# Kernel optimization log

Hardware: AMD Instinct MI355X
Metric: run time of the kernel (lower is better)

Reference implementation:

```python
import jax, jax.numpy as jnp
import numpy as np

E, K = 8, 2
B, S, H = 8, 2048, 512
R0, R1, O = 256, 256, 512
T = B * S


def _make_routing(key):
    # Mixtral-style: top-k softmax weights [T, K] and one-hot mask [E, K, T]
    k1, k2 = jax.random.split(key)
    sel = jax.random.randint(k1, (T, K), 0, E)                      # selected expert per (token, slot)
    rw = jax.nn.softmax(jax.random.normal(k2, (T, K)), axis=-1)
    mask = jax.nn.one_hot(sel, E, dtype=jnp.bool_)                  # [T, K, E]
    mask = jnp.transpose(mask, (2, 1, 0))                           # [E, K, T]
    return mask, rw


def setup_inputs() -> dict:
    key = jax.random.key(0)
    ks = jax.random.split(key, 10)
    x = jax.random.normal(ks[0], (B, S, H), dtype=jnp.float32)
    m1, rw1 = _make_routing(ks[1])
    m2, rw2 = _make_routing(ks[2])
    m3, rw3 = _make_routing(ks[3])
    s = 0.02
    W1 = jax.random.normal(ks[4], (E, R0, H), dtype=jnp.float32) * s
    b1 = jnp.zeros((E, R0), dtype=jnp.float32)
    W2 = jax.random.normal(ks[5], (E, R1, R0), dtype=jnp.float32) * s
    b2 = jnp.zeros((E, R1), dtype=jnp.float32)
    W3 = jax.random.normal(ks[6], (E, O, R1), dtype=jnp.float32) * s
    b3 = jnp.zeros((E, O), dtype=jnp.float32)
    return {"x": x,
            "expert_mask1": m1, "expert_mask2": m2, "expert_mask3": m3,
            "routing_weights1": rw1, "routing_weights2": rw2, "routing_weights3": rw3,
            "W1": W1, "b1": b1, "W2": W2, "b2": b2, "W3": W3, "b3": b3}


def _moe_stage(h, mask, rw, W, b, act):
    # combine[e, t] = routing weight of token t for expert e (0 if not routed)
    cmb = jnp.einsum('ekt,tk->et', mask.astype(h.dtype), rw)
    acc0 = jnp.zeros((h.shape[0], W.shape[1]), dtype=h.dtype)

    def body(acc, ew):
        Wi, bi, ci = ew            # Wi: [out, in], bi: [out], ci: [T]
        out = h @ Wi.T + bi
        if act:
            out = jax.nn.relu(out)
        return acc + ci[:, None] * out, None

    acc, _ = jax.lax.scan(body, acc0, (W, b, cmb))
    return acc


def reference(x, expert_mask1, expert_mask2, expert_mask3,
              routing_weights1, routing_weights2, routing_weights3,
              W1, b1, W2, b2, W3, b3):
    bsz, seq, dim = x.shape
    h = x.reshape(-1, dim)                                          # [T, H]
    h = _moe_stage(h, expert_mask1, routing_weights1, W1, b1, act=False)   # [T, R0]
    h = _moe_stage(h, expert_mask2, routing_weights2, W2, b2, act=False)   # [T, R1]
    h = _moe_stage(h, expert_mask3, routing_weights3, W3, b3, act=True)    # relu on expert output, then combine
    out = jax.nn.relu(h.reshape(bsz, seq, -1))
    return out
```

## Files before the change

kernel.cpp:

```cpp
#include <hip/hip_runtime.h>

#define T_TOKENS 16384
#define CAP 12288
#define CNT_STRIDE 16

typedef unsigned short u16;
typedef unsigned int u32;
typedef __attribute__((ext_vector_type(8))) short short8;
typedef __attribute__((ext_vector_type(4))) float float4v;

__device__ __forceinline__ u16 f2b(float f) {
  unsigned u = __float_as_uint(f);
  u = (u + 0x7fffu + ((u >> 16) & 1u)) >> 16;
  return (u16)u;
}
__device__ __forceinline__ float b2f(u16 h) {
  return __uint_as_float(((unsigned)h) << 16);
}

__device__ __forceinline__ void gl_lds16(const u16* g, u16* l) {
  __builtin_amdgcn_global_load_lds((const __attribute__((address_space(1))) u32*)g,
                                   (__attribute__((address_space(3))) u32*)l, 16, 0, 0);
}

__global__ __launch_bounds__(256) void prep_kernel(
    const int* __restrict__ m1, const int* __restrict__ m2, const int* __restrict__ m3,
    const float* __restrict__ rw1, const float* __restrict__ rw2, const float* __restrict__ rw3,
    const float* __restrict__ W1, const float* __restrict__ W2, const float* __restrict__ W3,
    u16* __restrict__ Wb1, u16* __restrict__ Wb2, u16* __restrict__ Wb3,
    int* __restrict__ cnt, int* __restrict__ idxbuf, float* __restrict__ wgtbuf) {
  const int tid = threadIdx.x;
  const int bid = blockIdx.x;
  if (bid < 64) {
    __shared__ int lcnt[24];
    __shared__ int lbase[24];
    if (tid < 24) lcnt[tid] = 0;
    __syncthreads();
    const int t = bid * 256 + tid;
    const int* masks[3] = {m1, m2, m3};
    const float* rws[3] = {rw1, rw2, rw3};
    int expert[3][2], lpos[3][2];
#pragma unroll
    for (int s = 0; s < 3; ++s)
#pragma unroll
      for (int k = 0; k < 2; ++k) {
        int e = 0;
#pragma unroll
        for (int j = 0; j < 8; ++j)
          if (masks[s][(j * 2 + k) * T_TOKENS + t] != 0) e = j;
        expert[s][k] = e;
        lpos[s][k] = atomicAdd(&lcnt[s * 8 + e], 1);
      }
    __syncthreads();
    if (tid < 24) lbase[tid] = atomicAdd(&cnt[tid * CNT_STRIDE], lcnt[tid]);
    __syncthreads();
#pragma unroll
    for (int s = 0; s < 3; ++s)
#pragma unroll
      for (int k = 0; k < 2; ++k) {
        int e = expert[s][k];
        int p = lbase[s * 8 + e] + lpos[s][k];
        if (p < CAP) {
          idxbuf[(s * 8 + e) * CAP + p] = t * 2 + k;
          wgtbuf[(s * 8 + e) * CAP + p] = rws[s][t * 2 + k];
        }
      }
  } else {
    for (int j = bid - 64; j < 1280; j += 192) {
      int base = j * 2048 + tid * 8;
      const float* src; u16* dst; int off = base;
      if (base < 1048576) { src = W1; dst = Wb1; }
      else if (base < 1572864) { src = W2; dst = Wb2; off = base - 1048576; }
      else { src = W3; dst = Wb3; off = base - 1572864; }
      float4 a0 = *(const float4*)(src + off);
      float4 a1 = *(const float4*)(src + off + 4);
      short8 v;
      v[0] = (short)f2b(a0.x); v[1] = (short)f2b(a0.y);
      v[2] = (short)f2b(a0.z); v[3] = (short)f2b(a0.w);
      v[4] = (short)f2b(a1.x); v[5] = (short)f2b(a1.y);
      v[6] = (short)f2b(a1.z); v[7] = (short)f2b(a1.w);
      *(short8*)(dst + off) = v;
    }
  }
}

template <int KDIM, int NDIM_TOTAL, int SRC, int RELU>
__global__ __launch_bounds__(256, 2) void moe_gemm(
    const void* __restrict__ Asrc_, const u16* __restrict__ Wb, const float* __restrict__ bias,
    const int* __restrict__ cnt, const int* __restrict__ idxbuf, const float* __restrict__ wgtbuf,
    u16* __restrict__ outTmp) {
  __shared__ __align__(16) u16 As[128 * 64];
  __shared__ __align__(16) u16 Bs[256 * 64];
  __shared__ int rowTok[128];
  __shared__ float rowW[128];

  int b = blockIdx.x;
  int e = -1, row0 = 0, n_e = 0, accb = 0;
#pragma unroll
  for (int j = 0; j < 8; ++j) {
    int nj = cnt[j * CNT_STRIDE];
    nj = nj > CAP ? CAP : nj;
    int nb = (nj + 127) >> 7;
    if (e < 0 && b < accb + nb) { e = j; row0 = (b - accb) << 7; n_e = nj; }
    accb += nb;
  }
  if (e < 0) return;

  const int tid = threadIdx.x;
  if (tid < 128) {
    int g = row0 + tid;
    bool ok = g < n_e;
    rowTok[tid] = ok ? idxbuf[e * CAP + g] : 0;
    rowW[tid] = ok ? wgtbuf[e * CAP + g] : 0.f;
  }
  __syncthreads();

  const int nbase = blockIdx.y * 256;
  const int wv = tid >> 6, lane = tid & 63;
  const int lrow = lane & 15, lquad = lane >> 4;
  const int mh = wv >> 1, nh = wv & 1;

  const u16* Wbe = Wb + ((size_t)e * NDIM_TOTAL + nbase) * KDIM;

  const int lr = lane >> 3;
  const int lgl = (lane & 7) ^ lr;
  const u16* gB = Wbe + (size_t)(wv * 8 + lr) * KDIM + lgl * 8;
  u16* lB = &Bs[(wv * 8) * 64];

  const float* ga_f[4];
  const u16* ga_b[4];
  int awoff[4];
#pragma unroll
  for (int i = 0; i < 4; ++i) {
    int r = i * 32 + (tid >> 3);
    if (SRC == 0)
      ga_f[i] = (const float*)Asrc_ + (size_t)(rowTok[r] >> 1) * KDIM + (tid & 7) * 8;
    else
      ga_b[i] = (const u16*)Asrc_ + (size_t)(rowTok[r] >> 1) * 2 * KDIM + (tid & 7) * 8;
    awoff[i] = (r * 8 + ((tid & 7) ^ (r & 7))) * 8;
  }

  float4v acc[4][8];
#pragma unroll
  for (int mt = 0; mt < 4; ++mt)
#pragma unroll
    for (int nt = 0; nt < 8; ++nt) acc[mt][nt] = (float4v)0.f;

  for (int kb = 0; kb < KDIM; kb += 64) {
#pragma unroll
    for (int i = 0; i < 8; ++i)
      gl_lds16(gB + (size_t)i * 32 * KDIM + kb, lB + i * 32 * 64);
    if (SRC == 0) {
#pragma unroll
      for (int i = 0; i < 4; ++i) {
        float4 a0 = *(const float4*)(ga_f[i] + kb);
        float4 a1 = *(const float4*)(ga_f[i] + kb + 4);
        short8 v;
        v[0] = (short)f2b(a0.x); v[1] = (short)f2b(a0.y);
        v[2] = (short)f2b(a0.z); v[3] = (short)f2b(a0.w);
        v[4] = (short)f2b(a1.x); v[5] = (short)f2b(a1.y);
        v[6] = (short)f2b(a1.z); v[7] = (short)f2b(a1.w);
        *(short8*)&As[awoff[i]] = v;
      }
    } else {
#pragma unroll
      for (int i = 0; i < 4; ++i) {
        short8 v0 = *(const short8*)(ga_b[i] + kb);
        short8 v1 = *(const short8*)(ga_b[i] + kb + KDIM);
        short8 v;
#pragma unroll
        for (int jj = 0; jj < 8; ++jj)
          v[jj] = (short)f2b(b2f((u16)v0[jj]) + b2f((u16)v1[jj]));
        *(short8*)&As[awoff[i]] = v;
      }
    }
    __syncthreads();
#pragma unroll
    for (int ks = 0; ks < 64; ks += 32) {
      const int gb = ks >> 3;
      short8 af[4], bf[8];
#pragma unroll
      for (int mt = 0; mt < 4; ++mt) {
        int r = mh * 64 + mt * 16 + lrow;
        int p = (gb + lquad) ^ (lrow & 7);
        af[mt] = *(const short8*)&As[(r * 8 + p) * 8];
      }
#pragma unroll
      for (int nt = 0; nt < 8; ++nt) {
        int r = nh * 128 + nt * 16 + lrow;
        int p = (gb + lquad) ^ (lrow & 7);
        bf[nt] = *(const short8*)&Bs[(r * 8 + p) * 8];
      }
#pragma unroll
      for (int mt = 0; mt < 4; ++mt)
#pragma unroll
        for (int nt = 0; nt < 8; ++nt)
          acc[mt][nt] = __builtin_amdgcn_mfma_f32_16x16x32_bf16(af[mt], bf[nt], acc[mt][nt], 0, 0, 0);
    }
    __syncthreads();
  }

  float bv[8];
#pragma unroll
  for (int nt = 0; nt < 8; ++nt)
    bv[nt] = bias[e * NDIM_TOTAL + nbase + nh * 128 + nt * 16 + lrow];
#pragma unroll
  for (int mt = 0; mt < 4; ++mt)
#pragma unroll
    for (int i = 0; i < 4; ++i) {
      int m = mh * 64 + mt * 16 + lquad * 4 + i;
      if (row0 + m < n_e) {
        float w = rowW[m];
        size_t drow = (size_t)rowTok[m] * NDIM_TOTAL + nbase + nh * 128;
#pragma unroll
        for (int nt = 0; nt < 8; ++nt) {
          float v = acc[mt][nt][i] + bv[nt];
          if (RELU) v = fmaxf(v, 0.f);
          outTmp[drow + nt * 16 + lrow] = f2b(v * w);
        }
      }
    }
}

__global__ void finalize_kernel(const u16* __restrict__ tmp3, float* __restrict__ out) {
  int f = (blockIdx.x * 256 + threadIdx.x) * 8;
  int t = f >> 9;
  int o = f & 511;
  const u16* p = tmp3 + (size_t)t * 1024 + o;
  short8 v0 = *(const short8*)p;
  short8 v1 = *(const short8*)(p + 512);
  float4 r0, r1;
  r0.x = fmaxf(b2f((u16)v0[0]) + b2f((u16)v1[0]), 0.f);
  r0.y = fmaxf(b2f((u16)v0[1]) + b2f((u16)v1[1]), 0.f);
  r0.z = fmaxf(b2f((u16)v0[2]) + b2f((u16)v1[2]), 0.f);
  r0.w = fmaxf(b2f((u16)v0[3]) + b2f((u16)v1[3]), 0.f);
  r1.x = fmaxf(b2f((u16)v0[4]) + b2f((u16)v1[4]), 0.f);
  r1.y = fmaxf(b2f((u16)v0[5]) + b2f((u16)v1[5]), 0.f);
  r1.z = fmaxf(b2f((u16)v0[6]) + b2f((u16)v1[6]), 0.f);
  r1.w = fmaxf(b2f((u16)v0[7]) + b2f((u16)v1[7]), 0.f);
  *(float4*)(out + f) = r0;
  *(float4*)(out + f + 4) = r1;
}

extern "C" void kernel_launch(void* const* d_in, const int* in_sizes, int n_in,
                              void* d_out, int out_size, void* d_ws, size_t ws_size,
                              hipStream_t stream) {
  const float* x  = (const float*)d_in[0];
  const int* m1   = (const int*)d_in[1];
  const int* m2   = (const int*)d_in[2];
  const int* m3   = (const int*)d_in[3];
  const float* rw1 = (const float*)d_in[4];
  const float* rw2 = (const float*)d_in[5];
  const float* rw3 = (const float*)d_in[6];
  const float* W1 = (const float*)d_in[7];
  const float* b1 = (const float*)d_in[8];
  const float* W2 = (const float*)d_in[9];
  const float* b2 = (const float*)d_in[10];
  const float* W3 = (const float*)d_in[11];
  const float* b3 = (const float*)d_in[12];
  float* out = (float*)d_out;

  char* ws = (char*)d_ws;
  size_t off = 0;
  int* cnt = (int*)(ws + off); off += 24 * CNT_STRIDE * 4;
  u16* Wb1 = (u16*)(ws + off); off += (size_t)8 * 256 * 512 * 2;
  u16* Wb2 = (u16*)(ws + off); off += (size_t)8 * 256 * 256 * 2;
  u16* Wb3 = (u16*)(ws + off); off += (size_t)8 * 512 * 256 * 2;
  u16* tmp1 = (u16*)(ws + off); off += (size_t)T_TOKENS * 2 * 256 * 2;
  u16* tmp2 = (u16*)(ws + off); off += (size_t)T_TOKENS * 2 * 256 * 2;
  u16* tmp3 = (u16*)(ws + off); off += (size_t)T_TOKENS * 2 * 512 * 2;
  int* idxb = (int*)(ws + off); off += (size_t)3 * 8 * CAP * 4;
  float* wgtb = (float*)(ws + off); off += (size_t)3 * 8 * CAP * 4;

  hipMemsetAsync(cnt, 0, 24 * CNT_STRIDE * 4, stream);
  prep_kernel<<<256, 256, 0, stream>>>(m1, m2, m3, rw1, rw2, rw3, W1, W2, W3,
                                       Wb1, Wb2, Wb3, cnt, idxb, wgtb);

  moe_gemm<512, 256, 0, 0><<<dim3(264, 1), 256, 0, stream>>>(
      x, Wb1, b1, cnt + 0, idxb + 0, wgtb + 0, tmp1);
  moe_gemm<256, 256, 1, 0><<<dim3(264, 1), 256, 0, stream>>>(
      tmp1, Wb2, b2, cnt + 8 * CNT_STRIDE, idxb + 8 * CAP, wgtb + 8 * CAP, tmp2);
  moe_gemm<256, 512, 1, 1><<<dim3(264, 2), 256, 0, stream>>>(
      tmp2, Wb3, b3, cnt + 16 * CNT_STRIDE, idxb + 16 * CAP, wgtb + 16 * CAP, tmp3);

  finalize_kernel<<<4096, 256, 0, stream>>>(tmp3, out);
}
```

Measured before the change: 193.1 us.

## Fuse three MoE GEMM stages and finalize into one persistent kernel

Replaces the three per-stage GEMM launches and the finalize launch with a single persistent kernel of 264 blocks. The blocks loop over jobs and synchronize between stages with atomic grid barriers. This removes launch gaps and tail effects between kernels. In exchange it adds barrier spin cost and relies on all 264 blocks being co-resident, and stage 3 now runs its 2x jobs over only 264 blocks in a loop.

```diff
diff --git a/kernel.cpp b/kernel.cpp
--- a/kernel.cpp
+++ b/kernel.cpp
@@ -3,6 +3,7 @@
 #define T_TOKENS 16384
 #define CAP 12288
 #define CNT_STRIDE 16
+#define GRID_MEGA 264
 
 typedef unsigned short u16;
 typedef unsigned int u32;
@@ -21,6 +22,17 @@
 __device__ __forceinline__ void gl_lds16(const u16* g, u16* l) {
   __builtin_amdgcn_global_load_lds((const __attribute__((address_space(1))) u32*)g,
                                    (__attribute__((address_space(3))) u32*)l, 16, 0, 0);
+}
+
+__device__ __forceinline__ void grid_barrier(int* bar, int nblk) {
+  __syncthreads();
+  if (threadIdx.x == 0) {
+    __threadfence();
+    __hip_atomic_fetch_add(bar, 1, __ATOMIC_ACQ_REL, __HIP_MEMORY_SCOPE_AGENT);
+    while (__hip_atomic_load(bar, __ATOMIC_ACQUIRE, __HIP_MEMORY_SCOPE_AGENT) < nblk)
+      __builtin_amdgcn_s_sleep(8);
+  }
+  __syncthreads();
 }
 
 __global__ __launch_bounds__(256) void prep_kernel(
@@ -85,161 +97,168 @@
 }
 
 template <int KDIM, int NDIM_TOTAL, int SRC, int RELU>
-__global__ __launch_bounds__(256, 2) void moe_gemm(
-    const void* __restrict__ Asrc_, const u16* __restrict__ Wb, const float* __restrict__ bias,
-    const int* __restrict__ cnt, const int* __restrict__ idxbuf, const float* __restrict__ wgtbuf,
-    u16* __restrict__ outTmp) {
+__device__ void gemm_stage(const void* __restrict__ Asrc_, const u16* __restrict__ Wb,
+                           const float* __restrict__ bias, const int* __restrict__ cnt,
+                           const int* __restrict__ idxbuf, const float* __restrict__ wgtbuf,
+                           u16* __restrict__ outTmp, u16* As, u16* Bs, int* rowTok, float* rowW) {
+  constexpr int NB = NDIM_TOTAL / 256;
+  const int tid = threadIdx.x;
+  const int wv = tid >> 6, lane = tid & 63;
+  const int lrow = lane & 15, lquad = lane >> 4;
+  const int mh = wv >> 1, nh = wv & 1;
+  const int lr = lane >> 3, lgl = (lane & 7) ^ lr;
+
+  int n_arr[8], nb_arr[8], tot = 0;
+#pragma unroll
+  for (int j = 0; j < 8; ++j) {
+    int nj = cnt[j * CNT_STRIDE];
+    nj = nj > CAP ? CAP : nj;
+    n_arr[j] = nj;
+    nb_arr[j] = (nj + 127) >> 7;
+    tot += nb_arr[j];
+  }
+  const int njobs = tot * NB;
+
+  for (int job = blockIdx.x; job < njobs; job += gridDim.x) {
+    int rb = job, nbase = 0;
+    if (NB == 2 && job >= tot) { rb = job - tot; nbase = 256; }
+    int ee = 0, row0 = 0, n_e = 0, a = 0;
+#pragma unroll
+    for (int j = 0; j < 8; ++j) {
+      if (rb >= a && rb < a + nb_arr[j]) { ee = j; row0 = (rb - a) << 7; n_e = n_arr[j]; }
+      a += nb_arr[j];
+    }
+    if (tid < 128) {
+      int g = row0 + tid;
+      bool ok = g < n_e;
+      rowTok[tid] = ok ? idxbuf[ee * CAP + g] : 0;
+      rowW[tid] = ok ? wgtbuf[ee * CAP + g] : 0.f;
+    }
+    __syncthreads();
+
+    const u16* Wbe = Wb + ((size_t)ee * NDIM_TOTAL + nbase) * KDIM;
+    const u16* gB = Wbe + (size_t)(wv * 8 + lr) * KDIM + lgl * 8;
+
+    float4v acc[4][8];
+#pragma unroll
+    for (int mt = 0; mt < 4; ++mt)
+#pragma unroll
+      for (int nt = 0; nt < 8; ++nt) acc[mt][nt] = (float4v)0.f;
+
+    for (int kb = 0; kb < KDIM; kb += 64) {
+#pragma unroll
+      for (int i = 0; i < 8; ++i)
+        gl_lds16(gB + (size_t)i * 32 * KDIM + kb, &Bs[(wv * 8 + i * 32) * 64]);
+#pragma unroll
+      for (int i = 0; i < 4; ++i) {
+        int row = i * 32 + (tid >> 3), lg = tid & 7, ph = lg ^ (row & 7);
+        short8 v;
+        if (SRC == 0) {
+          const float* xp = (const float*)Asrc_ + (size_t)(rowTok[row] >> 1) * KDIM + kb + lg * 8;
+          float4 a0 = *(const float4*)xp;
+          float4 a1 = *(const float4*)(xp + 4);
+          v[0] = (short)f2b(a0.x); v[1] = (short)f2b(a0.y);
+          v[2] = (short)f2b(a0.z); v[3] = (short)f2b(a0.w);
+          v[4] = (short)f2b(a1.x); v[5] = (short)f2b(a1.y);
+          v[6] = (short)f2b(a1.z); v[7] = (short)f2b(a1.w);
+        } else {
+          const u16* p0 = (const u16*)Asrc_ + (size_t)(rowTok[row] >> 1) * 2 * KDIM + kb + lg * 8;
+          short8 v0 = *(const short8*)p0;
+          short8 v1 = *(const short8*)(p0 + KDIM);
+#pragma unroll
+          for (int jj = 0; jj < 8; ++jj)
+            v[jj] = (short)f2b(b2f((u16)v0[jj]) + b2f((u16)v1[jj]));
+        }
+        *(short8*)&As[(row * 8 + ph) * 8] = v;
+      }
+      __syncthreads();
+#pragma unroll
+      for (int ks = 0; ks < 64; ks += 32) {
+        const int gb = ks >> 3;
+        short8 af[4], bf[8];
+#pragma unroll
+        for (int mt = 0; mt < 4; ++mt) {
+          int r = mh * 64 + mt * 16 + lrow;
+          int p = (gb + lquad) ^ (lrow & 7);
+          af[mt] = *(const short8*)&As[(r * 8 + p) * 8];
+        }
+#pragma unroll
+        for (int nt = 0; nt < 8; ++nt) {
+          int r = nh * 128 + nt * 16 + lrow;
+          int p = (gb + lquad) ^ (lrow & 7);
+          bf[nt] = *(const short8*)&Bs[(r * 8 + p) * 8];
+        }
+#pragma unroll
+        for (int mt = 0; mt < 4; ++mt)
+#pragma unroll
+          for (int nt = 0; nt < 8; ++nt)
+            acc[mt][nt] = __builtin_amdgcn_mfma_f32_16x16x32_bf16(af[mt], bf[nt], acc[mt][nt], 0, 0, 0);
+      }
+      __syncthreads();
+    }
+
+    float bv[8];
+#pragma unroll
+    for (int nt = 0; nt < 8; ++nt)
+      bv[nt] = bias[ee * NDIM_TOTAL + nbase + nh * 128 + nt * 16 + lrow];
+#pragma unroll
+    for (int mt = 0; mt < 4; ++mt)
+#pragma unroll
+      for (int i = 0; i < 4; ++i) {
+        int m = mh * 64 + mt * 16 + lquad * 4 + i;
+        if (row0 + m < n_e) {
+          float w = rowW[m];
+          size_t drow = (size_t)rowTok[m] * NDIM_TOTAL + nbase + nh * 128;
+#pragma unroll
+          for (int nt = 0; nt < 8; ++nt) {
+            float v = acc[mt][nt][i] + bv[nt];
+            if (RELU) v = fmaxf(v, 0.f);
+            outTmp[drow + nt * 16 + lrow] = f2b(v * w);
+          }
+        }
+      }
+    __syncthreads();
+  }
+}
+
+extern "C" __global__ void __launch_bounds__(256, 2) moe_mega(
+    const float* __restrict__ x, const float* __restrict__ b1, const float* __restrict__ b2,
+    const float* __restrict__ b3, float* __restrict__ out, int* __restrict__ cnt,
+    int* __restrict__ bars, u16* __restrict__ Wb1, u16* __restrict__ Wb2,
+    u16* __restrict__ Wb3, u16* __restrict__ tmp1, u16* __restrict__ tmp2,
+    u16* __restrict__ tmp3, int* __restrict__ idxb, float* __restrict__ wgtb) {
   __shared__ __align__(16) u16 As[128 * 64];
   __shared__ __align__(16) u16 Bs[256 * 64];
   __shared__ int rowTok[128];
   __shared__ float rowW[128];
 
-  int b = blockIdx.x;
-  int e = -1, row0 = 0, n_e = 0, accb = 0;
-#pragma unroll
-  for (int j = 0; j < 8; ++j) {
-    int nj = cnt[j * CNT_STRIDE];
-    nj = nj > CAP ? CAP : nj;
-    int nb = (nj + 127) >> 7;
-    if (e < 0 && b < accb + nb) { e = j; row0 = (b - accb) << 7; n_e = nj; }
-    accb += nb;
-  }
-  if (e < 0) return;
+  gemm_stage<512, 256, 0, 0>(x, Wb1, b1, cnt, idxb, wgtb, tmp1, As, Bs, rowTok, rowW);
+  grid_barrier(&bars[0], GRID_MEGA);
+  gemm_stage<256, 256, 1, 0>(tmp1, Wb2, b2, cnt + 8 * CNT_STRIDE, idxb + 8 * CAP,
+                             wgtb + 8 * CAP, tmp2, As, Bs, rowTok, rowW);
+  grid_barrier(&bars[1], GRID_MEGA);
+  gemm_stage<256, 512, 1, 1>(tmp2, Wb3, b3, cnt + 16 * CNT_STRIDE, idxb + 16 * CAP,
+                             wgtb + 16 * CAP, tmp3, As, Bs, rowTok, rowW);
+  grid_barrier(&bars[2], GRID_MEGA);
 
   const int tid = threadIdx.x;
-  if (tid < 128) {
-    int g = row0 + tid;
-    bool ok = g < n_e;
-    rowTok[tid] = ok ? idxbuf[e * CAP + g] : 0;
-    rowW[tid] = ok ? wgtbuf[e * CAP + g] : 0.f;
-  }
-  __syncthreads();
-
-  const int nbase = blockIdx.y * 256;
-  const int wv = tid >> 6, lane = tid & 63;
-  const int lrow = lane & 15, lquad = lane >> 4;
-  const int mh = wv >> 1, nh = wv & 1;
-
-  const u16* Wbe = Wb + ((size_t)e * NDIM_TOTAL + nbase) * KDIM;
-
-  const int lr = lane >> 3;
-  const int lgl = (lane & 7) ^ lr;
-  const u16* gB = Wbe + (size_t)(wv * 8 + lr) * KDIM + lgl * 8;
-  u16* lB = &Bs[(wv * 8) * 64];
-
-  const float* ga_f[4];
-  const u16* ga_b[4];
-  int awoff[4];
-#pragma unroll
-  for (int i = 0; i < 4; ++i) {
-    int r = i * 32 + (tid >> 3);
-    if (SRC == 0)
-      ga_f[i] = (const float*)Asrc_ + (size_t)(rowTok[r] >> 1) * KDIM + (tid & 7) * 8;
-    else
-      ga_b[i] = (const u16*)Asrc_ + (size_t)(rowTok[r] >> 1) * 2 * KDIM + (tid & 7) * 8;
-    awoff[i] = (r * 8 + ((tid & 7) ^ (r & 7))) * 8;
-  }
-
-  float4v acc[4][8];
-#pragma unroll
-  for (int mt = 0; mt < 4; ++mt)
-#pragma unroll
-    for (int nt = 0; nt < 8; ++nt) acc[mt][nt] = (float4v)0.f;
-
-  for (int kb = 0; kb < KDIM; kb += 64) {
-#pragma unroll
-    for (int i = 0; i < 8; ++i)
-      gl_lds16(gB + (size_t)i * 32 * KDIM + kb, lB + i * 32 * 64);
-    if (SRC == 0) {
-#pragma unroll
-      for (int i = 0; i < 4; ++i) {
-        float4 a0 = *(const float4*)(ga_f[i] + kb);
-        float4 a1 = *(const float4*)(ga_f[i] + kb + 4);
-        short8 v;
-        v[0] = (short)f2b(a0.x); v[1] = (short)f2b(a0.y);
-        v[2] = (short)f2b(a0.z); v[3] = (short)f2b(a0.w);
-        v[4] = (short)f2b(a1.x); v[5] = (short)f2b(a1.y);
-        v[6] = (short)f2b(a1.z); v[7] = (short)f2b(a1.w);
-        *(short8*)&As[awoff[i]] = v;
-      }
-    } else {
-#pragma unroll
-      for (int i = 0; i < 4; ++i) {
-        short8 v0 = *(const short8*)(ga_b[i] + kb);
-        short8 v1 = *(const short8*)(ga_b[i] + kb + KDIM);
-        short8 v;
-#pragma unroll
-        for (int jj = 0; jj < 8; ++jj)
-          v[jj] = (short)f2b(b2f((u16)v0[jj]) + b2f((u16)v1[jj]));
-        *(short8*)&As[awoff[i]] = v;
-      }
-    }
-    __syncthreads();
-#pragma unroll
-    for (int ks = 0; ks < 64; ks += 32) {
-      const int gb = ks >> 3;
-      short8 af[4], bf[8];
-#pragma unroll
-      for (int mt = 0; mt < 4; ++mt) {
-        int r = mh * 64 + mt * 16 + lrow;
-        int p = (gb + lquad) ^ (lrow & 7);
-        af[mt] = *(const short8*)&As[(r * 8 + p) * 8];
-      }
-#pragma unroll
-      for (int nt = 0; nt < 8; ++nt) {
-        int r = nh * 128 + nt * 16 + lrow;
-        int p = (gb + lquad) ^ (lrow & 7);
-        bf[nt] = *(const short8*)&Bs[(r * 8 + p) * 8];
-      }
-#pragma unroll
-      for (int mt = 0; mt < 4; ++mt)
-#pragma unroll
-        for (int nt = 0; nt < 8; ++nt)
-          acc[mt][nt] = __builtin_amdgcn_mfma_f32_16x16x32_bf16(af[mt], bf[nt], acc[mt][nt], 0, 0, 0);
-    }
-    __syncthreads();
-  }
-
-  float bv[8];
-#pragma unroll
-  for (int nt = 0; nt < 8; ++nt)
-    bv[nt] = bias[e * NDIM_TOTAL + nbase + nh * 128 + nt * 16 + lrow];
-#pragma unroll
-  for (int mt = 0; mt < 4; ++mt)
-#pragma unroll
-    for (int i = 0; i < 4; ++i) {
-      int m = mh * 64 + mt * 16 + lquad * 4 + i;
-      if (row0 + m < n_e) {
-        float w = rowW[m];
-        size_t drow = (size_t)rowTok[m] * NDIM_TOTAL + nbase + nh * 128;
-#pragma unroll
-        for (int nt = 0; nt < 8; ++nt) {
-          float v = acc[mt][nt][i] + bv[nt];
-          if (RELU) v = fmaxf(v, 0.f);
-          outTmp[drow + nt * 16 + lrow] = f2b(v * w);
-        }
-      }
-    }
-}
-
-__global__ void finalize_kernel(const u16* __restrict__ tmp3, float* __restrict__ out) {
-  int f = (blockIdx.x * 256 + threadIdx.x) * 8;
-  int t = f >> 9;
-  int o = f & 511;
-  const u16* p = tmp3 + (size_t)t * 1024 + o;
-  short8 v0 = *(const short8*)p;
-  short8 v1 = *(const short8*)(p + 512);
-  float4 r0, r1;
-  r0.x = fmaxf(b2f((u16)v0[0]) + b2f((u16)v1[0]), 0.f);
-  r0.y = fmaxf(b2f((u16)v0[1]) + b2f((u16)v1[1]), 0.f);
-  r0.z = fmaxf(b2f((u16)v0[2]) + b2f((u16)v1[2]), 0.f);
-  r0.w = fmaxf(b2f((u16)v0[3]) + b2f((u16)v1[3]), 0.f);
-  r1.x = fmaxf(b2f((u16)v0[4]) + b2f((u16)v1[4]), 0.f);
-  r1.y = fmaxf(b2f((u16)v0[5]) + b2f((u16)v1[5]), 0.f);
-  r1.z = fmaxf(b2f((u16)v0[6]) + b2f((u16)v1[6]), 0.f);
-  r1.w = fmaxf(b2f((u16)v0[7]) + b2f((u16)v1[7]), 0.f);
-  *(float4*)(out + f) = r0;
-  *(float4*)(out + f + 4) = r1;
+  for (int i = blockIdx.x * 256 + tid; i < T_TOKENS * 512 / 8; i += GRID_MEGA * 256) {
+    int f = i * 8, t = f >> 9, o = f & 511;
+    const u16* p = tmp3 + (size_t)t * 1024 + o;
+    short8 v0 = *(const short8*)p;
+    short8 v1 = *(const short8*)(p + 512);
+    float4 r0, r1;
+    r0.x = fmaxf(b2f((u16)v0[0]) + b2f((u16)v1[0]), 0.f);
+    r0.y = fmaxf(b2f((u16)v0[1]) + b2f((u16)v1[1]), 0.f);
+    r0.z = fmaxf(b2f((u16)v0[2]) + b2f((u16)v1[2]), 0.f);
+    r0.w = fmaxf(b2f((u16)v0[3]) + b2f((u16)v1[3]), 0.f);
+    r1.x = fmaxf(b2f((u16)v0[4]) + b2f((u16)v1[4]), 0.f);
+    r1.y = fmaxf(b2f((u16)v0[5]) + b2f((u16)v1[5]), 0.f);
+    r1.z = fmaxf(b2f((u16)v0[6]) + b2f((u16)v1[6]), 0.f);
+    r1.w = fmaxf(b2f((u16)v0[7]) + b2f((u16)v1[7]), 0.f);
+    *(float4*)(out + f) = r0;
+    *(float4*)(out + f + 4) = r1;
+  }
 }
 
 extern "C" void kernel_launch(void* const* d_in, const int* in_sizes, int n_in,
@@ -263,6 +282,7 @@
   char* ws = (char*)d_ws;
   size_t off = 0;
   int* cnt = (int*)(ws + off); off += 24 * CNT_STRIDE * 4;
+  int* bars = (int*)(ws + off); off += 16 * 4;
   u16* Wb1 = (u16*)(ws + off); off += (size_t)8 * 256 * 512 * 2;
   u16* Wb2 = (u16*)(ws + off); off += (size_t)8 * 256 * 256 * 2;
   u16* Wb3 = (u16*)(ws + off); off += (size_t)8 * 512 * 256 * 2;
@@ -272,16 +292,9 @@
   int* idxb = (int*)(ws + off); off += (size_t)3 * 8 * CAP * 4;
   float* wgtb = (float*)(ws + off); off += (size_t)3 * 8 * CAP * 4;
 
-  hipMemsetAsync(cnt, 0, 24 * CNT_STRIDE * 4, stream);
+  hipMemsetAsync(cnt, 0, (24 * CNT_STRIDE + 16) * 4, stream);
   prep_kernel<<<256, 256, 0, stream>>>(m1, m2, m3, rw1, rw2, rw3, W1, W2, W3,
                                        Wb1, Wb2, Wb3, cnt, idxb, wgtb);
-
-  moe_gemm<512, 256, 0, 0><<<dim3(264, 1), 256, 0, stream>>>(
-      x, Wb1, b1, cnt + 0, idxb + 0, wgtb + 0, tmp1);
-  moe_gemm<256, 256, 1, 0><<<dim3(264, 1), 256, 0, stream>>>(
-      tmp1, Wb2, b2, cnt + 8 * CNT_STRIDE, idxb + 8 * CAP, wgtb + 8 * CAP, tmp2);
-  moe_gemm<256, 512, 1, 1><<<dim3(264, 2), 256, 0, stream>>>(
-      tmp2, Wb3, b3, cnt + 16 * CNT_STRIDE, idxb + 16 * CAP, wgtb + 16 * CAP, tmp3);
-
-  finalize_kernel<<<4096, 256, 0, stream>>>(tmp3, out);
-}
+  moe_mega<<<GRID_MEGA, 256, 0, stream>>>(x, b1, b2, b3, out, cnt, bars,
+                                          Wb1, Wb2, Wb3, tmp1, tmp2, tmp3, idxb, wgtb);
+}
```

New measurement: 336.2 us. 74.1% more time.
